# Kernel tuning notes

Measured on AMD Instinct MI355X. Metric: run time of the kernel, lower is better.

The kernel has to match this reference:

```python
import jax, jax.numpy as jnp
import numpy as np

NEG_SLOPE = 0.2  # PyG GATv2Conv default negative_slope


def gatv2_conv(x, src, dst, edge_attr, Wl, bl, Wr, br, We, att, bias, H, C, N):
    """PyG GATv2Conv (concat=True, share_weights=False) with edge features.
    x: [N, F_in], src/dst: [E], edge_attr: [E, edge_dim]
    Wl/Wr: [F_in, H*C], We: [edge_dim, H*C], att: [H, C], bias: [H*C]
    Returns [N, H*C]."""
    xl = (x @ Wl + bl).reshape(N, H, C)   # source-side transform (x_j)
    xr = (x @ Wr + br).reshape(N, H, C)   # dest-side transform (x_i)
    e = (edge_attr @ We).reshape(-1, H, C)
    m = jax.nn.leaky_relu(xl[src] + xr[dst] + e, NEG_SLOPE)  # [E, H, C]
    alpha = jnp.einsum('ehc,hc->eh', m, att)                 # [E, H]
    # segment softmax over destination nodes
    amax = jax.ops.segment_max(alpha, dst, num_segments=N)   # [N, H]
    ex = jnp.exp(alpha - amax[dst])
    denom = jax.ops.segment_sum(ex, dst, num_segments=N)     # [N, H]
    a = ex / denom[dst]                                      # [E, H]
    out = jax.ops.segment_sum(xl[src] * a[:, :, None], dst, num_segments=N)
    return out.reshape(N, H * C) + bias


def setup_inputs() -> dict:
    key = jax.random.key(0)
    ks = jax.random.split(key, 24)
    N, E = 50000, 800000
    F_in, ED, HID, H, OUT = 32, 8, 64, 4, 256

    def w(k, shape, fan_in):
        return jax.random.normal(k, shape, dtype=jnp.float32) * (1.0 / np.sqrt(fan_in))

    x = jax.random.normal(ks[0], (N, F_in), dtype=jnp.float32)
    edge_index = jax.random.randint(ks[1], (2, E), 0, N, dtype=jnp.int64)
    edge_attr = jax.random.normal(ks[2], (E, ED), dtype=jnp.float32)
    return {
        'x': x, 'edge_index': edge_index, 'edge_attr': edge_attr,
        # MLP
        'W1': w(ks[3], (F_in, HID), F_in), 'b1': jnp.zeros((HID,), jnp.float32),
        'W2': w(ks[4], (HID, HID), HID), 'b2': jnp.zeros((HID,), jnp.float32),
        # gat1: in=HID, out=HID per head, heads=H
        'Wl1': w(ks[5], (HID, H * HID), HID), 'bl1': jnp.zeros((H * HID,), jnp.float32),
        'Wr1': w(ks[6], (HID, H * HID), HID), 'br1': jnp.zeros((H * HID,), jnp.float32),
        'We1': w(ks[7], (ED, H * HID), ED),
        'att1': w(ks[8], (H, HID), HID),
        'bias1': jnp.zeros((H * HID,), jnp.float32),
        # gat2: in=H*HID, out=OUT, heads=1
        'Wl2': w(ks[9], (H * HID, OUT), H * HID), 'bl2': jnp.zeros((OUT,), jnp.float32),
        'Wr2': w(ks[10], (H * HID, OUT), H * HID), 'br2': jnp.zeros((OUT,), jnp.float32),
        'We2': w(ks[11], (ED, OUT), ED),
        'att2': w(ks[12], (1, OUT), OUT),
        'bias2': jnp.zeros((OUT,), jnp.float32),
    }


def reference(x, edge_index, edge_attr, W1, b1, W2, b2,
              Wl1, bl1, Wr1, br1, We1, att1, bias1,
              Wl2, bl2, Wr2, br2, We2, att2, bias2):
    N = x.shape[0]
    H, HID, OUT = 4, 64, 256
    src, dst = edge_index[0], edge_index[1]
    # MLP encoder
    h = jax.nn.relu(x @ W1 + b1)
    h = jax.nn.relu(h @ W2 + b2)
    # GAT layer 1 (4 heads, concat) + ReLU (dropout is identity at inference)
    h = gatv2_conv(h, src, dst, edge_attr, Wl1, bl1, Wr1, br1, We1, att1, bias1, H, HID, N)
    h = jax.nn.relu(h)
    # GAT layer 2 (1 head) + ReLU
    h = gatv2_conv(h, src, dst, edge_attr, Wl2, bl2, Wr2, br2, We2, att2, bias2, 1, OUT, N)
    return jax.nn.relu(h)
```

## Files before the change

### kernel.cpp

```cpp
#include <hip/hip_runtime.h>
#include <hip/hip_bf16.h>
#include <math.h>

#define LR_SLOPE 0.2f

typedef __attribute__((ext_vector_type(8))) short bf16x8;
typedef __attribute__((ext_vector_type(4))) float f32x4;
typedef __attribute__((ext_vector_type(2))) float f32x2;

__device__ __forceinline__ unsigned short f2bf(float f) {
    unsigned u = __float_as_uint(f);
    u = (u + 0x7FFFu + ((u >> 16) & 1u)) >> 16;
    return (unsigned short)u;
}

__device__ __forceinline__ f32x2 bf2f2(unsigned u) {
    f32x2 r;
    r.x = __uint_as_float(u << 16);
    r.y = __uint_as_float(u & 0xffff0000u);
    return r;
}

__device__ __forceinline__ f32x2 pk_fma(f32x2 a, f32x2 b, f32x2 c) {
    return __builtin_elementwise_fma(a, b, c);
}
__device__ __forceinline__ f32x2 pk_max(f32x2 a, f32x2 b) {
    return __builtin_elementwise_max(a, b);
}

template <int CTRL>
__device__ __forceinline__ float add_dpp(float v) {
    const int r = __builtin_amdgcn_update_dpp(0, __float_as_int(v),
                                              CTRL, 0xF, 0xF, true);
    return v + __int_as_float(r);
}

__global__ __launch_bounds__(256) void gemm_bias_act(
    const float* __restrict__ A, const float* __restrict__ W,
    const float* __restrict__ bias, float* __restrict__ outf,
    short* __restrict__ outb, int M, int N, int K, int do_relu)
{
    __shared__ float As[16][64];
    __shared__ float Ws[16][64];
    const int tid = threadIdx.x;
    const int tx = tid & 15;
    const int ty = tid >> 4;
    const int row0 = blockIdx.x * 64;
    const int col0 = blockIdx.y * 64;

    float acc[4][4] = {{0.f}};

    for (int kk = 0; kk < K; kk += 16) {
        {
            const int ra = tid >> 2;
            const int ka = (tid & 3) << 2;
            float4 v = make_float4(0.f, 0.f, 0.f, 0.f);
            const int r = row0 + ra;
            if (r < M)
                v = *reinterpret_cast<const float4*>(&A[(size_t)r * K + kk + ka]);
            As[ka + 0][ra] = v.x;
            As[ka + 1][ra] = v.y;
            As[ka + 2][ra] = v.z;
            As[ka + 3][ra] = v.w;
        }
        {
            const int rw = tid >> 4;
            const int cw = (tid & 15) << 2;
            float4 v = *reinterpret_cast<const float4*>(
                &W[(size_t)(kk + rw) * N + col0 + cw]);
            *reinterpret_cast<float4*>(&Ws[rw][cw]) = v;
        }
        __syncthreads();
#pragma unroll
        for (int k = 0; k < 16; ++k) {
            const float4 a = *reinterpret_cast<const float4*>(&As[k][ty * 4]);
            const float4 b = *reinterpret_cast<const float4*>(&Ws[k][tx * 4]);
            const float av[4] = {a.x, a.y, a.z, a.w};
            const float bv[4] = {b.x, b.y, b.z, b.w};
#pragma unroll
            for (int i = 0; i < 4; ++i)
#pragma unroll
                for (int j = 0; j < 4; ++j)
                    acc[i][j] += av[i] * bv[j];
        }
        __syncthreads();
    }

    const int cbase = col0 + tx * 4;
#pragma unroll
    for (int i = 0; i < 4; ++i) {
        const int r = row0 + ty * 4 + i;
        if (r >= M) continue;
        float v[4];
#pragma unroll
        for (int j = 0; j < 4; ++j) {
            v[j] = acc[i][j] + bias[cbase + j];
            if (do_relu) v[j] = fmaxf(v[j], 0.f);
        }
        if (outb) {
            short4 s;
            s.x = (short)f2bf(v[0]); s.y = (short)f2bf(v[1]);
            s.z = (short)f2bf(v[2]); s.w = (short)f2bf(v[3]);
            *reinterpret_cast<short4*>(&outb[(size_t)r * N + cbase]) = s;
        } else {
            float4 o; o.x = v[0]; o.y = v[1]; o.z = v[2]; o.w = v[3];
            *reinterpret_cast<float4*>(&outf[(size_t)r * N + cbase]) = o;
        }
    }
}

__global__ void wtrans_all_k(
    const float* __restrict__ Wl1, const float* __restrict__ Wr1,
    const float* __restrict__ Wl2, const float* __restrict__ Wr2,
    short* __restrict__ o1, short* __restrict__ o2,
    short* __restrict__ o3, short* __restrict__ o4)
{
    const int i = blockIdx.x * 256 + threadIdx.x;
    const int S1 = 256 * 64, S2 = 256 * 256;
    if (i < S1) {
        const int n = i / 64, k = i % 64;
        o1[i] = (short)f2bf(Wl1[(size_t)k * 256 + n]);
    } else if (i < 2 * S1) {
        const int j = i - S1;
        const int n = j / 64, k = j % 64;
        o2[j] = (short)f2bf(Wr1[(size_t)k * 256 + n]);
    } else if (i < 2 * S1 + S2) {
        const int j = i - 2 * S1;
        const int n = j / 256, k = j % 256;
        o3[j] = (short)f2bf(Wl2[(size_t)k * 256 + n]);
    } else if (i < 2 * S1 + 2 * S2) {
        const int j = i - 2 * S1 - S2;
        const int n = j / 256, k = j % 256;
        o4[j] = (short)f2bf(Wr2[(size_t)k * 256 + n]);
    }
}

__global__ __launch_bounds__(256) void gemm_mfma_dual(
    const short* __restrict__ A,
    const short* __restrict__ Wt0, const float* __restrict__ b0,
    short* __restrict__ out0,
    const short* __restrict__ Wt1, const float* __restrict__ b1,
    short* __restrict__ out1,
    int M, int N, int K)
{
    const short* __restrict__ Wt   = blockIdx.z ? Wt1 : Wt0;
    const float* __restrict__ bias = blockIdx.z ? b1 : b0;
    short* __restrict__ out        = blockIdx.z ? out1 : out0;

    __shared__ __align__(16) short As[4][128][8];
    __shared__ __align__(16) short Bs[4][128][8];

    const int tid = threadIdx.x;
    const int lane = tid & 63;
    const int wid = tid >> 6;
    const int wm = wid >> 1, wn = wid & 1;
    const int row0 = blockIdx.x * 128;
    const int col0 = blockIdx.y * 128;

    f32x4 acc[4][4] = {};

    const int srow = tid & 127;
    const int skg2 = tid >> 7;

    for (int kk = 0; kk < K; kk += 32) {
        {
            const int r = row0 + srow;
            bf16x8 a0 = {0, 0, 0, 0, 0, 0, 0, 0};
            bf16x8 a1 = {0, 0, 0, 0, 0, 0, 0, 0};
            if (r < M) {
                const bf16x8* p = reinterpret_cast<const bf16x8*>(
                    &A[(size_t)r * K + kk + skg2 * 16]);
                a0 = p[0]; a1 = p[1];
            }
            *reinterpret_cast<bf16x8*>(&As[skg2 * 2 + 0][srow][0]) = a0;
            *reinterpret_cast<bf16x8*>(&As[skg2 * 2 + 1][srow][0]) = a1;
        }
        {
            const float4* p = reinterpret_cast<const float4*>(
                &Wt[(size_t)(col0 + srow) * K + kk + skg2 * 16]);
            *reinterpret_cast<float4*>(&Bs[skg2 * 2 + 0][srow][0]) = p[0];
            *reinterpret_cast<float4*>(&Bs[skg2 * 2 + 1][srow][0]) = p[1];
        }
        __syncthreads();

        const int kg = lane >> 4, li = lane & 15;
        bf16x8 af[4], bfr[4];
#pragma unroll
        for (int mi = 0; mi < 4; ++mi)
            af[mi] = *reinterpret_cast<bf16x8*>(&As[kg][wm * 64 + mi * 16 + li][0]);
#pragma unroll
        for (int ni = 0; ni < 4; ++ni)
            bfr[ni] = *reinterpret_cast<bf16x8*>(&Bs[kg][wn * 64 + ni * 16 + li][0]);
#pragma unroll
        for (int mi = 0; mi < 4; ++mi)
#pragma unroll
            for (int ni = 0; ni < 4; ++ni)
                acc[mi][ni] = __builtin_amdgcn_mfma_f32_16x16x32_bf16(
                    af[mi], bfr[ni], acc[mi][ni], 0, 0, 0);
        __syncthreads();
    }

    const int li = lane & 15, lq = lane >> 4;
#pragma unroll
    for (int ni = 0; ni < 4; ++ni) {
        const int c = col0 + wn * 64 + ni * 16 + li;
        const float bv = bias[c];
#pragma unroll
        for (int mi = 0; mi < 4; ++mi) {
#pragma unroll
            for (int r = 0; r < 4; ++r) {
                const int row = row0 + wm * 64 + mi * 16 + lq * 4 + r;
                if (row < M)
                    out[(size_t)row * N + c] = (short)f2bf(acc[mi][ni][r] + bv);
            }
        }
    }
}

__global__ void hist_k(const int* __restrict__ dst, int* __restrict__ deg, int E)
{
    const int e = blockIdx.x * blockDim.x + threadIdx.x;
    if (e < E) atomicAdd(&deg[dst[e]], 1);
}

__global__ void scan1_k(const int* __restrict__ deg, int* __restrict__ rowptr,
                        int* __restrict__ bsum, int N)
{
    __shared__ int buf[256];
    const int i = blockIdx.x * 256 + threadIdx.x;
    const int v = (i < N) ? deg[i] : 0;
    buf[threadIdx.x] = v;
    __syncthreads();
#pragma unroll
    for (int off = 1; off < 256; off <<= 1) {
        const int t = (threadIdx.x >= (unsigned)off) ? buf[threadIdx.x - off] : 0;
        __syncthreads();
        buf[threadIdx.x] += t;
        __syncthreads();
    }
    if (i < N) rowptr[i] = buf[threadIdx.x] - v;
    if (threadIdx.x == 255) bsum[blockIdx.x] = buf[255];
}

__global__ void scan2_k(int* __restrict__ bsum, int nb)
{
    __shared__ int buf[256];
    const int v = (threadIdx.x < (unsigned)nb) ? bsum[threadIdx.x] : 0;
    buf[threadIdx.x] = v;
    __syncthreads();
#pragma unroll
    for (int off = 1; off < 256; off <<= 1) {
        const int t = (threadIdx.x >= (unsigned)off) ? buf[threadIdx.x - off] : 0;
        __syncthreads();
        buf[threadIdx.x] += t;
        __syncthreads();
    }
    if (threadIdx.x < (unsigned)nb) bsum[threadIdx.x] = buf[threadIdx.x] - v;
}

__global__ void scan3_k(int* __restrict__ rowptr, const int* __restrict__ bsum,
                        int* __restrict__ cursor, int N, int E)
{
    const int i = blockIdx.x * 256 + threadIdx.x;
    if (i < N) {
        const int r = rowptr[i] + bsum[blockIdx.x];
        rowptr[i] = r;
        cursor[i] = r;
    }
    if (i == 0) rowptr[N] = E;
}

__global__ void scatter_k(const int* __restrict__ src, const int* __restrict__ dst,
                          const float4* __restrict__ eattr,
                          int* __restrict__ cursor,
                          int* __restrict__ ssrc, float4* __restrict__ ea_s, int E)
{
    const int e = blockIdx.x * blockDim.x + threadIdx.x;
    if (e >= E) return;
    const int d = dst[e];
    const int p = atomicAdd(&cursor[d], 1);
    ssrc[p] = src[e];
    const float4 e0 = eattr[2 * e];
    const float4 e1 = eattr[2 * e + 1];
    ea_s[2 * p] = e0;
    ea_s[2 * p + 1] = e1;
}

template <int H, int NPW, int OB>
__global__ __launch_bounds__(256, 4) void node_gat_k(
    const short* __restrict__ xl, const short* __restrict__ xr,
    const float4* __restrict__ ea_s, const int* __restrict__ ssrc,
    const float* __restrict__ We, const float* __restrict__ att,
    const float* __restrict__ bias,
    const int* __restrict__ rowptr, void* __restrict__ outv, int N)
{
    const int lane = threadIdx.x & 63;
    const int nbase = (blockIdx.x * 4 + (threadIdx.x >> 6)) * NPW;
    if (nbase >= N) return;

    const int hc0 = (H == 4) ? (((lane >> 4) << 6) + ((lane & 15) << 2))
                             : (lane << 2);

    f32x2 we2[8][2];
#pragma unroll
    for (int t = 0; t < 8; ++t) {
        const float4 v = *reinterpret_cast<const float4*>(&We[t * 256 + hc0]);
        we2[t][0] = (f32x2){v.x, v.y};
        we2[t][1] = (f32x2){v.z, v.w};
    }
    const float4 a4 = *reinterpret_cast<const float4*>(&att[hc0]);
    const f32x2 av2[2] = {(f32x2){a4.x, a4.y}, (f32x2){a4.z, a4.w}};
    const float4 b4 = *reinterpret_cast<const float4*>(&bias[hc0]);
    const f32x2 bv2[2] = {(f32x2){b4.x, b4.y}, (f32x2){b4.z, b4.w}};

    for (int ni = 0; ni < NPW; ++ni) {
        const int n = nbase + ni;
        if (n >= N) return;
        const uint2 rp = *reinterpret_cast<const uint2*>(
            &xr[(unsigned)((n << 8) + hc0)]);
        const f32x2 xrv2[2] = {bf2f2(rp.x), bf2f2(rp.y)};

        f32x2 acc2[2] = {(f32x2){0.f, 0.f}, (f32x2){0.f, 0.f}};
        float m = -INFINITY, den = 0.f;

        const int k0 = __builtin_amdgcn_readfirstlane(rowptr[n]);
        const int k1 = __builtin_amdgcn_readfirstlane(rowptr[n + 1]);

        auto load_e = [&](const int ks, f32x2 (&xv)[2], float (&ea)[8]) {
            const int sv = ssrc[ks];
            const short* xp = xl + ((unsigned)sv << 8);
            const uint2 xpv = *reinterpret_cast<const uint2*>(xp + hc0);
            xv[0] = bf2f2(xpv.x);
            xv[1] = bf2f2(xpv.y);
            const float4 e0 = ea_s[2 * ks];
            const float4 e1 = ea_s[2 * ks + 1];
            ea[0] = e0.x; ea[1] = e0.y; ea[2] = e0.z; ea[3] = e0.w;
            ea[4] = e1.x; ea[5] = e1.y; ea[6] = e1.z; ea[7] = e1.w;
        };
        auto sc_of = [&](const f32x2 (&xv)[2], const float (&ea)[8]) -> float {
            f32x2 p2 = {0.f, 0.f};
#pragma unroll
            for (int q = 0; q < 2; ++q) {
                f32x2 s = xv[q] + xrv2[q];
#pragma unroll
                for (int t = 0; t < 8; ++t)
                    s = pk_fma((f32x2){ea[t], ea[t]}, we2[t][q], s);
                s = pk_max(s, s * LR_SLOPE);
                p2 = pk_fma(s, av2[q], p2);
            }
            float p = p2.x + p2.y;
            p = add_dpp<0x121>(p);
            p = add_dpp<0x122>(p);
            p = add_dpp<0x124>(p);
            p = add_dpp<0x128>(p);
            if (H == 1) {
                p += __int_as_float(__builtin_amdgcn_ds_swizzle(
                         __float_as_int(p), 0x401F));
                p += __shfl_xor(p, 32, 64);
            }
            return p;
        };

        int k = k0;
        for (; k + 4 <= k1; k += 4) {
            f32x2 x0[2], x1[2], x2[2], x3[2];
            float ea0[8], ea1[8], ea2[8], ea3[8];
            load_e(k, x0, ea0);     load_e(k + 1, x1, ea1);
            load_e(k + 2, x2, ea2); load_e(k + 3, x3, ea3);
            const float s0 = sc_of(x0, ea0);
            const float s1 = sc_of(x1, ea1);
            const float s2 = sc_of(x2, ea2);
            const float s3 = sc_of(x3, ea3);
            const float nm = fmaxf(fmaxf(m, fmaxf(s0, s1)), fmaxf(s2, s3));
            const float sc = __expf(m - nm);
            const float w0 = __expf(s0 - nm), w1 = __expf(s1 - nm);
            const float w2 = __expf(s2 - nm), w3 = __expf(s3 - nm);
            den = fmaf(den, sc, (w0 + w1) + (w2 + w3));
            const f32x2 scv = {sc, sc};
            const f32x2 w0v = {w0, w0}, w1v = {w1, w1};
            const f32x2 w2v = {w2, w2}, w3v = {w3, w3};
#pragma unroll
            for (int q = 0; q < 2; ++q)
                acc2[q] = pk_fma(acc2[q], scv,
                          pk_fma(w0v, x0[q],
                          pk_fma(w1v, x1[q],
                          pk_fma(w2v, x2[q], w3v * x3[q]))));
            m = nm;
        }
        for (; k < k1; ++k) {
            f32x2 x0[2]; float ea0[8];
            load_e(k, x0, ea0);
            const float s0 = sc_of(x0, ea0);
            const float nm = fmaxf(m, s0);
            const float sc = __expf(m - nm);
            const float w0 = __expf(s0 - nm);
            den = fmaf(den, sc, w0);
            const f32x2 scv = {sc, sc};
            const f32x2 w0v = {w0, w0};
#pragma unroll
            for (int q = 0; q < 2; ++q)
                acc2[q] = pk_fma(acc2[q], scv, w0v * x0[q]);
            m = nm;
        }

        const float inv = (den > 0.f) ? 1.f / den : 0.f;
        const f32x2 invv = {inv, inv};
        const f32x2 z2 = {0.f, 0.f};
        const f32x2 o0 = pk_max(pk_fma(acc2[0], invv, bv2[0]), z2);
        const f32x2 o1 = pk_max(pk_fma(acc2[1], invv, bv2[1]), z2);
        if (OB) {
            short4 s;
            s.x = (short)f2bf(o0.x); s.y = (short)f2bf(o0.y);
            s.z = (short)f2bf(o1.x); s.w = (short)f2bf(o1.y);
            *reinterpret_cast<short4*>(
                &((short*)outv)[(unsigned)((n << 8) + hc0)]) = s;
        } else {
            float4 o; o.x = o0.x; o.y = o0.y; o.z = o1.x; o.w = o1.y;
            *reinterpret_cast<float4*>(
                &((float*)outv)[(unsigned)((n << 8) + hc0)]) = o;
        }
    }
}

extern "C" void kernel_launch(void* const* d_in, const int* in_sizes, int n_in,
                              void* d_out, int out_size, void* d_ws, size_t ws_size,
                              hipStream_t stream)
{
    const float* x     = (const float*)d_in[0];
    const int*   eidx  = (const int*)d_in[1];
    const float* eattr = (const float*)d_in[2];
    const float* W1  = (const float*)d_in[3];
    const float* b1  = (const float*)d_in[4];
    const float* W2  = (const float*)d_in[5];
    const float* b2  = (const float*)d_in[6];
    const float* Wl1 = (const float*)d_in[7];
    const float* bl1 = (const float*)d_in[8];
    const float* Wr1 = (const float*)d_in[9];
    const float* br1 = (const float*)d_in[10];
    const float* We1 = (const float*)d_in[11];
    const float* att1 = (const float*)d_in[12];
    const float* bias1 = (const float*)d_in[13];
    const float* Wl2 = (const float*)d_in[14];
    const float* bl2 = (const float*)d_in[15];
    const float* Wr2 = (const float*)d_in[16];
    const float* br2 = (const float*)d_in[17];
    const float* We2 = (const float*)d_in[18];
    const float* att2 = (const float*)d_in[19];
    const float* bias2 = (const float*)d_in[20];

    const int N = in_sizes[0] / 32;
    const int E = in_sizes[2] / 8;
    const int* src = eidx;
    const int* dst = eidx + E;

    auto align256 = [](size_t v) { return (v + 255) & ~(size_t)255; };
    char* ws = (char*)d_ws;
    size_t off = 0;
    float* h1 = (float*)(ws + off);    off += align256((size_t)N * 64 * 4);
    short* h2b = (short*)(ws + off);   off += align256((size_t)N * 64 * 4);
    float4* ea_s = (float4*)h1;
    short* xl = (short*)(ws + off);    off += align256((size_t)N * 256 * 2);
    short* xr = (short*)(ws + off);    off += align256((size_t)N * 256 * 2);
    short* out1b = (short*)(ws + off); off += align256((size_t)N * 256 * 2);
    int* deg = (int*)(ws + off);       off += align256((size_t)N * 4);
    int* rowptr = (int*)(ws + off);    off += align256((size_t)(N + 1) * 4);
    int* cursor = (int*)(ws + off);    off += align256((size_t)N * 4);
    int* bsum = (int*)(ws + off);      off += align256((size_t)1024 * 4);
    int* ssrc = (int*)(ws + off);      off += align256((size_t)E * 4);
    short* wtl1 = (short*)(ws + off);  off += align256((size_t)256 * 64 * 2);
    short* wtr1 = (short*)(ws + off);  off += align256((size_t)256 * 64 * 2);
    short* wtl2 = (short*)(ws + off);  off += align256((size_t)256 * 256 * 2);
    short* wtr2 = (short*)(ws + off);  off += align256((size_t)256 * 256 * 2);
    (void)ws_size;

    float* outf = (float*)d_out;

    const int egrid1 = (E + 255) / 256;
    const int nblk = (N + 255) / 256;
    const int NPW = 4;
    const int ngat = (N + 4 * NPW - 1) / (4 * NPW);

    wtrans_all_k<<<(2 * 256 * 64 + 2 * 256 * 256 + 255) / 256, 256, 0, stream>>>(
        Wl1, Wr1, Wl2, Wr2, wtl1, wtr1, wtl2, wtr2);

    {
        dim3 g1((N + 63) / 64, 1);
        gemm_bias_act<<<g1, 256, 0, stream>>>(x,  W1, b1, h1, nullptr, N, 64, 32, 1);
        gemm_bias_act<<<g1, 256, 0, stream>>>(h1, W2, b2, nullptr, h2b, N, 64, 64, 1);
    }

    {
        dim3 g((N + 127) / 128, 2, 2);
        gemm_mfma_dual<<<g, 256, 0, stream>>>(h2b, wtl1, bl1, xl, wtr1, br1, xr,
                                              N, 256, 64);
    }

    hipMemsetAsync(deg, 0, (size_t)N * 4, stream);
    hist_k<<<egrid1, 256, 0, stream>>>(dst, deg, E);
    scan1_k<<<nblk, 256, 0, stream>>>(deg, rowptr, bsum, N);
    scan2_k<<<1, 256, 0, stream>>>(bsum, nblk);
    scan3_k<<<nblk, 256, 0, stream>>>(rowptr, bsum, cursor, N, E);
    scatter_k<<<egrid1, 256, 0, stream>>>(src, dst, (const float4*)eattr,
                                          cursor, ssrc, ea_s, E);

    node_gat_k<4, NPW, 1><<<ngat, 256, 0, stream>>>(xl, xr, ea_s, ssrc,
                                                    We1, att1, bias1,
                                                    rowptr, out1b, N);

    {
        dim3 g((N + 127) / 128, 2, 2);
        gemm_mfma_dual<<<g, 256, 0, stream>>>(out1b, wtl2, bl2, xl, wtr2, br2, xr,
                                              N, 256, 256);
    }

    node_gat_k<1, NPW, 0><<<ngat, 256, 0, stream>>>(xl, xr, ea_s, ssrc,
                                                    We2, att2, bias2,
                                                    rowptr, outf, N);
}
```

Measured before the change: 427.7 us.

## Fuse two MLP GEMMs into one kernel and double-buffer edge loads in GAT

Replaces the two separate gemm_bias_act launches with one fused kernel that keeps the first layer's output tile in shared memory and writes only the bf16 second-layer result. This removes the global round trip of the fp32 intermediate and one launch. The node GAT edge loop now prefetches the next group of four edges while computing the current group, to hide gather latency. The prefetch raises register pressure. The workspace layout changes so that ea_s gets its own buffer instead of aliasing h1.

```diff
diff --git a/kernel.cpp b/kernel.cpp
--- a/kernel.cpp
+++ b/kernel.cpp
@@ -35,77 +35,109 @@
     return v + __int_as_float(r);
 }
 
-__global__ __launch_bounds__(256) void gemm_bias_act(
-    const float* __restrict__ A, const float* __restrict__ W,
-    const float* __restrict__ bias, float* __restrict__ outf,
-    short* __restrict__ outb, int M, int N, int K, int do_relu)
-{
-    __shared__ float As[16][64];
-    __shared__ float Ws[16][64];
+__global__ __launch_bounds__(256) void fused_mlp_k(
+    const float* __restrict__ x,
+    const float* __restrict__ W1,
+    const float* __restrict__ b1,
+    const float* __restrict__ W2,
+    const float* __restrict__ b2,
+    short* __restrict__ h2b,
+    int M)
+{
+    __shared__ float smem[4096 + 64 * 68];
+    float* As  = smem;
+    float* Ws  = smem + 2048;
+    float* Hs  = smem + 4096;
+    float* Ws2 = smem;
+
     const int tid = threadIdx.x;
     const int tx = tid & 15;
     const int ty = tid >> 4;
     const int row0 = blockIdx.x * 64;
-    const int col0 = blockIdx.y * 64;
+
+    {
+        const int r = tid >> 2;
+        const int c = (tid & 3) * 8;
+        const int row = row0 + r;
+        float v[8] = {0.f, 0.f, 0.f, 0.f, 0.f, 0.f, 0.f, 0.f};
+        if (row < M) {
+            *reinterpret_cast<float4*>(&v[0]) =
+                *reinterpret_cast<const float4*>(&x[(size_t)row * 32 + c]);
+            *reinterpret_cast<float4*>(&v[4]) =
+                *reinterpret_cast<const float4*>(&x[(size_t)row * 32 + c + 4]);
+        }
+#pragma unroll
+        for (int j = 0; j < 8; ++j) As[(c + j) * 64 + r] = v[j];
+    }
+    {
+        const int e0 = tid * 8;
+        *reinterpret_cast<float4*>(&Ws[e0]) =
+            *reinterpret_cast<const float4*>(&W1[e0]);
+        *reinterpret_cast<float4*>(&Ws[e0 + 4]) =
+            *reinterpret_cast<const float4*>(&W1[e0 + 4]);
+    }
+    __syncthreads();
 
     float acc[4][4] = {{0.f}};
-
-    for (int kk = 0; kk < K; kk += 16) {
-        {
-            const int ra = tid >> 2;
-            const int ka = (tid & 3) << 2;
-            float4 v = make_float4(0.f, 0.f, 0.f, 0.f);
-            const int r = row0 + ra;
-            if (r < M)
-                v = *reinterpret_cast<const float4*>(&A[(size_t)r * K + kk + ka]);
-            As[ka + 0][ra] = v.x;
-            As[ka + 1][ra] = v.y;
-            As[ka + 2][ra] = v.z;
-            As[ka + 3][ra] = v.w;
-        }
-        {
-            const int rw = tid >> 4;
-            const int cw = (tid & 15) << 2;
-            float4 v = *reinterpret_cast<const float4*>(
-                &W[(size_t)(kk + rw) * N + col0 + cw]);
-            *reinterpret_cast<float4*>(&Ws[rw][cw]) = v;
-        }
-        __syncthreads();
-#pragma unroll
-        for (int k = 0; k < 16; ++k) {
-            const float4 a = *reinterpret_cast<const float4*>(&As[k][ty * 4]);
-            const float4 b = *reinterpret_cast<const float4*>(&Ws[k][tx * 4]);
-            const float av[4] = {a.x, a.y, a.z, a.w};
-            const float bv[4] = {b.x, b.y, b.z, b.w};
-#pragma unroll
-            for (int i = 0; i < 4; ++i)
-#pragma unroll
-                for (int j = 0; j < 4; ++j)
-                    acc[i][j] += av[i] * bv[j];
-        }
-        __syncthreads();
-    }
-
-    const int cbase = col0 + tx * 4;
+#pragma unroll
+    for (int k = 0; k < 32; ++k) {
+        float a[4], b[4];
+        *reinterpret_cast<float4*>(a) =
+            *reinterpret_cast<const float4*>(&As[k * 64 + ty * 4]);
+        *reinterpret_cast<float4*>(b) =
+            *reinterpret_cast<const float4*>(&Ws[k * 64 + tx * 4]);
+#pragma unroll
+        for (int i = 0; i < 4; ++i)
+#pragma unroll
+            for (int j = 0; j < 4; ++j)
+                acc[i][j] = fmaf(a[i], b[j], acc[i][j]);
+    }
+#pragma unroll
+    for (int j = 0; j < 4; ++j) {
+        const float bj = b1[tx * 4 + j];
+#pragma unroll
+        for (int i = 0; i < 4; ++i)
+            Hs[(tx * 4 + j) * 68 + ty * 4 + i] = fmaxf(acc[i][j] + bj, 0.f);
+    }
+    __syncthreads();
+
+    {
+        const int e0 = tid * 16;
+#pragma unroll
+        for (int q = 0; q < 4; ++q)
+            *reinterpret_cast<float4*>(&Ws2[e0 + q * 4]) =
+                *reinterpret_cast<const float4*>(&W2[e0 + q * 4]);
+    }
+    __syncthreads();
+
+    float acc2[4][4] = {{0.f}};
+#pragma unroll
+    for (int k = 0; k < 64; ++k) {
+        float a[4], b[4];
+        *reinterpret_cast<float4*>(a) =
+            *reinterpret_cast<const float4*>(&Hs[k * 68 + ty * 4]);
+        *reinterpret_cast<float4*>(b) =
+            *reinterpret_cast<const float4*>(&Ws2[k * 64 + tx * 4]);
+#pragma unroll
+        for (int i = 0; i < 4; ++i)
+#pragma unroll
+            for (int j = 0; j < 4; ++j)
+                acc2[i][j] = fmaf(a[i], b[j], acc2[i][j]);
+    }
+    const int cbase = tx * 4;
+    float bv[4];
+    *reinterpret_cast<float4*>(bv) =
+        *reinterpret_cast<const float4*>(&b2[cbase]);
 #pragma unroll
     for (int i = 0; i < 4; ++i) {
-        const int r = row0 + ty * 4 + i;
-        if (r >= M) continue;
-        float v[4];
-#pragma unroll
-        for (int j = 0; j < 4; ++j) {
-            v[j] = acc[i][j] + bias[cbase + j];
-            if (do_relu) v[j] = fmaxf(v[j], 0.f);
-        }
-        if (outb) {
-            short4 s;
-            s.x = (short)f2bf(v[0]); s.y = (short)f2bf(v[1]);
-            s.z = (short)f2bf(v[2]); s.w = (short)f2bf(v[3]);
-            *reinterpret_cast<short4*>(&outb[(size_t)r * N + cbase]) = s;
-        } else {
-            float4 o; o.x = v[0]; o.y = v[1]; o.z = v[2]; o.w = v[3];
-            *reinterpret_cast<float4*>(&outf[(size_t)r * N + cbase]) = o;
-        }
+        const int row = row0 + ty * 4 + i;
+        if (row >= M) continue;
+        short4 s;
+        s.x = (short)f2bf(fmaxf(acc2[i][0] + bv[0], 0.f));
+        s.y = (short)f2bf(fmaxf(acc2[i][1] + bv[1], 0.f));
+        s.z = (short)f2bf(fmaxf(acc2[i][2] + bv[2], 0.f));
+        s.w = (short)f2bf(fmaxf(acc2[i][3] + bv[3], 0.f));
+        *reinterpret_cast<short4*>(&h2b[(size_t)row * 64 + cbase]) = s;
     }
 }
 
@@ -360,17 +392,15 @@
             }
             return p;
         };
-
-        int k = k0;
-        for (; k + 4 <= k1; k += 4) {
-            f32x2 x0[2], x1[2], x2[2], x3[2];
-            float ea0[8], ea1[8], ea2[8], ea3[8];
-            load_e(k, x0, ea0);     load_e(k + 1, x1, ea1);
-            load_e(k + 2, x2, ea2); load_e(k + 3, x3, ea3);
-            const float s0 = sc_of(x0, ea0);
-            const float s1 = sc_of(x1, ea1);
-            const float s2 = sc_of(x2, ea2);
-            const float s3 = sc_of(x3, ea3);
+        auto loadG = [&](const int kb, f32x2 (&xv)[4][2], float (&ea)[4][8]) {
+#pragma unroll
+            for (int e = 0; e < 4; ++e) load_e(kb + e, xv[e], ea[e]);
+        };
+        auto computeG = [&](const f32x2 (&xv)[4][2], const float (&ea)[4][8]) {
+            const float s0 = sc_of(xv[0], ea[0]);
+            const float s1 = sc_of(xv[1], ea[1]);
+            const float s2 = sc_of(xv[2], ea[2]);
+            const float s3 = sc_of(xv[3], ea[3]);
             const float nm = fmaxf(fmaxf(m, fmaxf(s0, s1)), fmaxf(s2, s3));
             const float sc = __expf(m - nm);
             const float w0 = __expf(s0 - nm), w1 = __expf(s1 - nm);
@@ -382,10 +412,29 @@
 #pragma unroll
             for (int q = 0; q < 2; ++q)
                 acc2[q] = pk_fma(acc2[q], scv,
-                          pk_fma(w0v, x0[q],
-                          pk_fma(w1v, x1[q],
-                          pk_fma(w2v, x2[q], w3v * x3[q]))));
+                          pk_fma(w0v, xv[0][q],
+                          pk_fma(w1v, xv[1][q],
+                          pk_fma(w2v, xv[2][q], w3v * xv[3][q]))));
             m = nm;
+        };
+
+        f32x2 xA[4][2], xB[4][2];
+        float eaA[4][8], eaB[4][8];
+
+        int k = k0;
+        const int ng = (k1 - k0) >> 2;
+        if (ng > 0) {
+            loadG(k, xA, eaA);
+            int g = 0;
+            for (; g + 2 <= ng; g += 2) {
+                loadG(k + 4, xB, eaB);
+                computeG(xA, eaA);
+                if (g + 2 < ng)
+                    loadG(k + 8, xA, eaA);
+                computeG(xB, eaB);
+                k += 8;
+            }
+            if (ng & 1) { computeG(xA, eaA); k += 4; }
         }
         for (; k < k1; ++k) {
             f32x2 x0[2]; float ea0[8];
@@ -456,9 +505,8 @@
     auto align256 = [](size_t v) { return (v + 255) & ~(size_t)255; };
     char* ws = (char*)d_ws;
     size_t off = 0;
-    float* h1 = (float*)(ws + off);    off += align256((size_t)N * 64 * 4);
-    short* h2b = (short*)(ws + off);   off += align256((size_t)N * 64 * 4);
-    float4* ea_s = (float4*)h1;
+    short* h2b = (short*)(ws + off);   off += align256((size_t)N * 64 * 2);
+    float4* ea_s = (float4*)(ws + off); off += align256((size_t)E * 32);
     short* xl = (short*)(ws + off);    off += align256((size_t)N * 256 * 2);
     short* xr = (short*)(ws + off);    off += align256((size_t)N * 256 * 2);
     short* out1b = (short*)(ws + off); off += align256((size_t)N * 256 * 2);
@@ -483,11 +531,7 @@
     wtrans_all_k<<<(2 * 256 * 64 + 2 * 256 * 256 + 255) / 256, 256, 0, stream>>>(
         Wl1, Wr1, Wl2, Wr2, wtl1, wtr1, wtl2, wtr2);
 
-    {
-        dim3 g1((N + 63) / 64, 1);
-        gemm_bias_act<<<g1, 256, 0, stream>>>(x,  W1, b1, h1, nullptr, N, 64, 32, 1);
-        gemm_bias_act<<<g1, 256, 0, stream>>>(h1, W2, b2, nullptr, h2b, N, 64, 64, 1);
-    }
+    fused_mlp_k<<<(N + 63) / 64, 256, 0, stream>>>(x, W1, b1, W2, b2, h2b, N);
 
     {
         dim3 g((N + 127) / 128, 2, 2);
```

Result: slower. 536.1 us (+25.3%).
